# Kernel tuning notes

Measured on AMD Instinct MI355X. Metric: run time of the kernel, lower is better.

## Reference

```python
import jax, jax.numpy as jnp
import numpy as np

NUM_CLASSES = 256
WEIGHT = 0.0005
EPS = 1e-12  # torch F.normalize eps


def setup_inputs() -> dict:
    key = jax.random.key(0)
    k1, k2 = jax.random.split(key)
    features = jax.random.normal(k1, (32768, 1024), dtype=jnp.float32)
    labels = jax.random.randint(k2, (32768,), 0, NUM_CLASSES, dtype=jnp.int32)
    return {"features": features, "labels": labels}


def _centroid_loss(features, labels):
    B, D = features.shape
    # row-wise L2 normalize (torch F.normalize: x / max(||x||, eps))
    norms = jnp.linalg.norm(features, axis=1, keepdims=True)
    f = features / jnp.maximum(norms, EPS)

    ones = jnp.ones((B,), f.dtype)
    counts = jax.ops.segment_sum(ones, labels, num_segments=NUM_CLASSES)  # [C]
    sums = jax.ops.segment_sum(f, labels, num_segments=NUM_CLASSES)       # [C, D]

    # rank of each sample within its class (order of first appearance),
    # matching the row order of features[class_mask] in the original loop
    onehot = jax.nn.one_hot(labels, NUM_CLASSES, dtype=jnp.int32)          # [B, C]
    rank = jnp.take_along_axis(jnp.cumsum(onehot, axis=0), labels[:, None].astype(jnp.int32), axis=1)[:, 0] - 1

    # idx_table[c, r] = global index of the r-th member of class c; sentinel B if none
    idx_table = jnp.full((NUM_CLASSES, B), B, dtype=jnp.int32)
    idx_table = idx_table.at[labels, rank].set(jnp.arange(B, dtype=jnp.int32))

    # NOTE: the original code indexes class_features with the GLOBAL index i
    # (arange(n_c) != i), i.e. it excludes the member of the class at position i,
    # and excludes nothing when i >= n_c. We reproduce that exactly.
    arange_b = jnp.arange(B)
    k = idx_table[labels, arange_b]            # class member at in-class position i (global i)
    valid_excl = k < B                          # exclusion only happens when i < class size
    excl_feat = jnp.where(valid_excl[:, None], f[jnp.where(valid_excl, k, 0)], 0.0)

    n_c = counts[labels]                        # class size per sample (float)
    denom = jnp.where(valid_excl, n_c - 1.0, n_c)
    denom = jnp.maximum(denom, 1.0)             # safe for masked-out singleton classes
    centroid = (sums[labels] - excl_feat) / denom[:, None]

    dist = jnp.mean((f - centroid) ** 2, axis=1)  # F.mse_loss(..., reduction='mean')
    contrib = jnp.where(n_c > 1.0, dist, 0.0)     # skip classes with <=1 sample
    return WEIGHT * jnp.sum(contrib) / B


def reference(features, labels):
    return _centroid_loss(features, labels)
```

## Files before the change

kernel.cpp:

```cpp
#include <hip/hip_runtime.h>

#define BN 32768
#define DN 1024
#define CN 256
#define RCAP 320

__device__ __forceinline__ float dot4(float4 a, float4 b) {
    return a.x*b.x + a.y*b.y + a.z*b.z + a.w*b.w;
}

__global__ void __launch_bounds__(256) k_norm(const float4* __restrict__ x4,
                                              float* __restrict__ rnorm) {
    const int lane = threadIdx.x & 63;
    const int gw = (int)((blockIdx.x * 256u + threadIdx.x) >> 6);
    for (int row = gw; row < BN; row += 8192) {
        const float4* b4 = x4 + (size_t)row * 256;
        const float4 v0 = b4[lane];
        const float4 v1 = b4[lane + 64];
        const float4 v2 = b4[lane + 128];
        const float4 v3 = b4[lane + 192];
        float ss = dot4(v0, v0) + dot4(v1, v1) + dot4(v2, v2) + dot4(v3, v3);
#pragma unroll
        for (int off = 32; off; off >>= 1) ss += __shfl_xor(ss, off, 64);
        if (lane == 0) rnorm[row] = 1.0f / fmaxf(sqrtf(ss), 1e-12f);
    }
}

__global__ void __launch_bounds__(1024) k_acc(const float4* __restrict__ x4,
                                              const int* __restrict__ labels,
                                              const float* __restrict__ rnorm,
                                              float* __restrict__ out) {
    __shared__ unsigned int packed[BN / 4];
    __shared__ int sic[RCAP];
    __shared__ float rnl[RCAP];
    __shared__ int wcnt[16];
    __shared__ float fa[(DN / 4) * 5];
    __shared__ float wred[4];
    __shared__ float4 cred[4];

    const int c = blockIdx.x;
    const int t = threadIdx.x;

    for (int w = t; w < BN / 4; w += 1024) {
        const int4 v = ((const int4*)labels)[w];
        packed[w] = (unsigned int)(v.x & 255)
                  | ((unsigned int)(v.y & 255) << 8)
                  | ((unsigned int)(v.z & 255) << 16)
                  | ((unsigned int)(v.w & 255) << 24);
    }
    for (int i = t; i < (DN / 4) * 5; i += 1024) fa[i] = 0.0f;
    __syncthreads();

    const int wave = t >> 6, lane = t & 63;
    const unsigned long long lt = (lane == 0) ? 0ull : (~0ull >> (64 - lane));
    const int ch0 = wave * 32, ch1 = ch0 + 32;

    int cnt = 0;
    for (int ch = ch0; ch < ch1; ++ch) {
        const int gi = ch * 64 + lane;
        const int lab = (packed[gi >> 2] >> ((gi & 3) * 8)) & 255;
        cnt += __popcll(__ballot(lab == c));
    }
    if (lane == 0) wcnt[wave] = cnt;
    __syncthreads();

    int base = 0, ntot = 0;
    for (int w2 = 0; w2 < 16; ++w2) {
        const int v = wcnt[w2];
        if (w2 < wave) base += v;
        ntot += v;
    }

    for (int ch = ch0; ch < ch1; ++ch) {
        const int gi = ch * 64 + lane;
        const int lab = (packed[gi >> 2] >> ((gi & 3) * 8)) & 255;
        const bool pred = (lab == c);
        const unsigned long long mask = __ballot(pred);
        if (pred) {
            const int pos = base + __popcll(mask & lt);
            if (pos < RCAP) {
                sic[pos] = gi;
                rnl[pos] = rnorm[gi];
            }
        }
        base += __popcll(mask);
    }
    __syncthreads();

    const int nn = min(ntot, RCAP);
    float4 a0 = make_float4(0.f, 0.f, 0.f, 0.f), a1 = a0, a2 = a0, a3 = a0;
    for (int r = wave; r < nn; r += 32) {
        const int rowA = sic[r];
        const float rnA = rnl[r];
        const bool hasB = (r + 16) < nn;
        const int rowB = hasB ? sic[r + 16] : rowA;
        const float rnB = hasB ? rnl[r + 16] : 0.0f;
        const float4* bA = x4 + (size_t)rowA * 256;
        const float4* bB = x4 + (size_t)rowB * 256;
        const float4 uA0 = bA[lane];
        const float4 uA1 = bA[lane + 64];
        const float4 uA2 = bA[lane + 128];
        const float4 uA3 = bA[lane + 192];
        const float4 uB0 = bB[lane];
        const float4 uB1 = bB[lane + 64];
        const float4 uB2 = bB[lane + 128];
        const float4 uB3 = bB[lane + 192];
        a0.x += uA0.x * rnA + uB0.x * rnB; a0.y += uA0.y * rnA + uB0.y * rnB;
        a0.z += uA0.z * rnA + uB0.z * rnB; a0.w += uA0.w * rnA + uB0.w * rnB;
        a1.x += uA1.x * rnA + uB1.x * rnB; a1.y += uA1.y * rnA + uB1.y * rnB;
        a1.z += uA1.z * rnA + uB1.z * rnB; a1.w += uA1.w * rnA + uB1.w * rnB;
        a2.x += uA2.x * rnA + uB2.x * rnB; a2.y += uA2.y * rnA + uB2.y * rnB;
        a2.z += uA2.z * rnA + uB2.z * rnB; a2.w += uA2.w * rnA + uB2.w * rnB;
        a3.x += uA3.x * rnA + uB3.x * rnB; a3.y += uA3.y * rnA + uB3.y * rnB;
        a3.z += uA3.z * rnA + uB3.z * rnB; a3.w += uA3.w * rnA + uB3.w * rnB;
    }

    {
        const int q0 = lane, q1 = lane + 64, q2 = lane + 128, q3 = lane + 192;
        atomicAdd(&fa[5 * q0 + 0], a0.x); atomicAdd(&fa[5 * q0 + 1], a0.y);
        atomicAdd(&fa[5 * q0 + 2], a0.z); atomicAdd(&fa[5 * q0 + 3], a0.w);
        atomicAdd(&fa[5 * q1 + 0], a1.x); atomicAdd(&fa[5 * q1 + 1], a1.y);
        atomicAdd(&fa[5 * q1 + 2], a1.z); atomicAdd(&fa[5 * q1 + 3], a1.w);
        atomicAdd(&fa[5 * q2 + 0], a2.x); atomicAdd(&fa[5 * q2 + 1], a2.y);
        atomicAdd(&fa[5 * q2 + 2], a2.z); atomicAdd(&fa[5 * q2 + 3], a2.w);
        atomicAdd(&fa[5 * q3 + 0], a3.x); atomicAdd(&fa[5 * q3 + 1], a3.y);
        atomicAdd(&fa[5 * q3 + 2], a3.z); atomicAdd(&fa[5 * q3 + 3], a3.w);
    }
    __syncthreads();

    float4 Sq = make_float4(0.f, 0.f, 0.f, 0.f);
    float d = 0.0f;
    if (t < 256) {
        Sq.x = fa[5 * t + 0]; Sq.y = fa[5 * t + 1];
        Sq.z = fa[5 * t + 2]; Sq.w = fa[5 * t + 3];
        d = dot4(Sq, Sq);
    }
    if (wave < 4) {
#pragma unroll
        for (int off = 32; off; off >>= 1) d += __shfl_xor(d, off, 64);
        if (lane == 0) wred[wave] = d;
    }
    __syncthreads();

    const int n = ntot;
    if (n >= 2) {
        const float s2 = wred[0] + wred[1] + wred[2] + wred[3];
        const int nlim = min(n, nn);
        float dacc = 0.0f;
        for (int p = 0; p < nn; ++p) {
            const int j = sic[p];
            if (j >= nlim) continue;
            const int k = sic[j];
            if (t < 256) {
                const float4 xi = x4[(size_t)j * 256 + t];
                const float4 xk = x4[(size_t)k * 256 + t];
                float d0 = dot4(xi, Sq);
                float d1 = dot4(xi, xk);
                float d2 = dot4(xk, Sq);
                float d3 = dot4(xk, xk);
#pragma unroll
                for (int off = 32; off; off >>= 1) {
                    d0 += __shfl_xor(d0, off, 64);
                    d1 += __shfl_xor(d1, off, 64);
                    d2 += __shfl_xor(d2, off, 64);
                    d3 += __shfl_xor(d3, off, 64);
                }
                if (lane == 0) cred[wave] = make_float4(d0, d1, d2, d3);
            }
            __syncthreads();
            if (t == 0) {
                const float xiS  = cred[0].x + cred[1].x + cred[2].x + cred[3].x;
                const float xixk = cred[0].y + cred[1].y + cred[2].y + cred[3].y;
                const float xkS  = cred[0].z + cred[1].z + cred[2].z + cred[3].z;
                const float xkxk = cred[0].w + cred[1].w + cred[2].w + cred[3].w;
                const float rni = rnl[p];
                const float rnk = rnl[j];
                const float fiS  = rni * xiS;
                const float fifk = rni * rnk * xixk;
                const float Sfk  = rnk * xkS;
                const float fk2  = rnk * rnk * xkxk;
                const float nf = (float)n;
                const float dd = nf - 1.0f;
                const float naive = -2.0f * fiS / nf + s2 / (nf * nf);
                const float corr  = -2.0f * (fiS - fifk) / dd
                                  + (s2 - 2.0f * Sfk + fk2) / (dd * dd);
                dacc += corr - naive;
            }
            __syncthreads();
        }
        if (t == 0) {
            const float nf = (float)n;
            const float total = (nf - s2 / nf) + dacc;
            atomicAdd(out, total * (1.0f / DN) * (0.0005f / (float)BN));
        }
    }
}

extern "C" void kernel_launch(void* const* d_in, const int* in_sizes, int n_in,
                              void* d_out, int out_size, void* d_ws, size_t ws_size,
                              hipStream_t stream) {
    const float4* x4 = (const float4*)d_in[0];
    const int* labels = (const int*)d_in[1];
    float* out = (float*)d_out;

    float* rnorm = (float*)d_ws;

    hipMemsetAsync(out, 0, sizeof(float), stream);
    k_norm<<<2048, 256, 0, stream>>>(x4, rnorm);
    k_acc<<<CN, 1024, 0, stream>>>(x4, labels, rnorm, out);
}
```

Before: 242.2 us.

## Fuse row-norm computation into per-class accumulation kernel and cache ballot masks

Drops the separate normalisation kernel. Each class block now computes the inverse L2 norm of each member row while it loads that row to accumulate the class sum, so the features are read from global memory once fewer times and the workspace round-trip for the norms goes away. Ballot masks from the counting pass are stored in shared memory and reused in the compaction pass instead of re-decoding labels. The accumulation loop now loads one row per wave per iteration instead of two, which lowers memory-level parallelism per wave. Norm work is also spread over only 256 blocks instead of a grid-wide kernel.

Result: faster. 227.5 us (-6.1%).

```diff
diff --git a/kernel.cpp b/kernel.cpp
--- a/kernel.cpp
+++ b/kernel.cpp
@@ -9,28 +9,11 @@
     return a.x*b.x + a.y*b.y + a.z*b.z + a.w*b.w;
 }
 
-__global__ void __launch_bounds__(256) k_norm(const float4* __restrict__ x4,
-                                              float* __restrict__ rnorm) {
-    const int lane = threadIdx.x & 63;
-    const int gw = (int)((blockIdx.x * 256u + threadIdx.x) >> 6);
-    for (int row = gw; row < BN; row += 8192) {
-        const float4* b4 = x4 + (size_t)row * 256;
-        const float4 v0 = b4[lane];
-        const float4 v1 = b4[lane + 64];
-        const float4 v2 = b4[lane + 128];
-        const float4 v3 = b4[lane + 192];
-        float ss = dot4(v0, v0) + dot4(v1, v1) + dot4(v2, v2) + dot4(v3, v3);
-#pragma unroll
-        for (int off = 32; off; off >>= 1) ss += __shfl_xor(ss, off, 64);
-        if (lane == 0) rnorm[row] = 1.0f / fmaxf(sqrtf(ss), 1e-12f);
-    }
-}
-
-__global__ void __launch_bounds__(1024) k_acc(const float4* __restrict__ x4,
+__global__ void __launch_bounds__(1024) k_all(const float4* __restrict__ x4,
                                               const int* __restrict__ labels,
-                                              const float* __restrict__ rnorm,
                                               float* __restrict__ out) {
     __shared__ unsigned int packed[BN / 4];
+    __shared__ unsigned long long smask[BN / 64];
     __shared__ int sic[RCAP];
     __shared__ float rnl[RCAP];
     __shared__ int wcnt[16];
@@ -59,7 +42,9 @@
     for (int ch = ch0; ch < ch1; ++ch) {
         const int gi = ch * 64 + lane;
         const int lab = (packed[gi >> 2] >> ((gi & 3) * 8)) & 255;
-        cnt += __popcll(__ballot(lab == c));
+        const unsigned long long mask = __ballot(lab == c);
+        if (lane == 0) smask[ch] = mask;
+        cnt += __popcll(mask);
     }
     if (lane == 0) wcnt[wave] = cnt;
     __syncthreads();
@@ -72,16 +57,10 @@
     }
 
     for (int ch = ch0; ch < ch1; ++ch) {
-        const int gi = ch * 64 + lane;
-        const int lab = (packed[gi >> 2] >> ((gi & 3) * 8)) & 255;
-        const bool pred = (lab == c);
-        const unsigned long long mask = __ballot(pred);
-        if (pred) {
+        const unsigned long long mask = smask[ch];
+        if ((mask >> lane) & 1ull) {
             const int pos = base + __popcll(mask & lt);
-            if (pos < RCAP) {
-                sic[pos] = gi;
-                rnl[pos] = rnorm[gi];
-            }
+            if (pos < RCAP) sic[pos] = ch * 64 + lane;
         }
         base += __popcll(mask);
     }
@@ -89,30 +68,22 @@
 
     const int nn = min(ntot, RCAP);
     float4 a0 = make_float4(0.f, 0.f, 0.f, 0.f), a1 = a0, a2 = a0, a3 = a0;
-    for (int r = wave; r < nn; r += 32) {
-        const int rowA = sic[r];
-        const float rnA = rnl[r];
-        const bool hasB = (r + 16) < nn;
-        const int rowB = hasB ? sic[r + 16] : rowA;
-        const float rnB = hasB ? rnl[r + 16] : 0.0f;
-        const float4* bA = x4 + (size_t)rowA * 256;
-        const float4* bB = x4 + (size_t)rowB * 256;
-        const float4 uA0 = bA[lane];
-        const float4 uA1 = bA[lane + 64];
-        const float4 uA2 = bA[lane + 128];
-        const float4 uA3 = bA[lane + 192];
-        const float4 uB0 = bB[lane];
-        const float4 uB1 = bB[lane + 64];
-        const float4 uB2 = bB[lane + 128];
-        const float4 uB3 = bB[lane + 192];
-        a0.x += uA0.x * rnA + uB0.x * rnB; a0.y += uA0.y * rnA + uB0.y * rnB;
-        a0.z += uA0.z * rnA + uB0.z * rnB; a0.w += uA0.w * rnA + uB0.w * rnB;
-        a1.x += uA1.x * rnA + uB1.x * rnB; a1.y += uA1.y * rnA + uB1.y * rnB;
-        a1.z += uA1.z * rnA + uB1.z * rnB; a1.w += uA1.w * rnA + uB1.w * rnB;
-        a2.x += uA2.x * rnA + uB2.x * rnB; a2.y += uA2.y * rnA + uB2.y * rnB;
-        a2.z += uA2.z * rnA + uB2.z * rnB; a2.w += uA2.w * rnA + uB2.w * rnB;
-        a3.x += uA3.x * rnA + uB3.x * rnB; a3.y += uA3.y * rnA + uB3.y * rnB;
-        a3.z += uA3.z * rnA + uB3.z * rnB; a3.w += uA3.w * rnA + uB3.w * rnB;
+    for (int r = wave; r < nn; r += 16) {
+        const int row = sic[r];
+        const float4* b4 = x4 + (size_t)row * 256;
+        const float4 v0 = b4[lane];
+        const float4 v1 = b4[lane + 64];
+        const float4 v2 = b4[lane + 128];
+        const float4 v3 = b4[lane + 192];
+        float ss = dot4(v0, v0) + dot4(v1, v1) + dot4(v2, v2) + dot4(v3, v3);
+#pragma unroll
+        for (int off = 32; off; off >>= 1) ss += __shfl_xor(ss, off, 64);
+        const float rn = 1.0f / fmaxf(sqrtf(ss), 1e-12f);
+        if (lane == 0) rnl[r] = rn;
+        a0.x += v0.x * rn; a0.y += v0.y * rn; a0.z += v0.z * rn; a0.w += v0.w * rn;
+        a1.x += v1.x * rn; a1.y += v1.y * rn; a1.z += v1.z * rn; a1.w += v1.w * rn;
+        a2.x += v2.x * rn; a2.y += v2.y * rn; a2.z += v2.z * rn; a2.w += v2.w * rn;
+        a3.x += v3.x * rn; a3.y += v3.y * rn; a3.z += v3.z * rn; a3.w += v3.w * rn;
     }
 
     {
@@ -203,9 +174,6 @@
     const int* labels = (const int*)d_in[1];
     float* out = (float*)d_out;
 
-    float* rnorm = (float*)d_ws;
-
     hipMemsetAsync(out, 0, sizeof(float), stream);
-    k_norm<<<2048, 256, 0, stream>>>(x4, rnorm);
-    k_acc<<<CN, 1024, 0, stream>>>(x4, labels, rnorm, out);
+    k_all<<<CN, 1024, 0, stream>>>(x4, labels, out);
 }
```
